# Kernel optimization log

Hardware: AMD Instinct MI355X
Metric: run time of the kernel (lower is better)

## Reference

```python
import jax, jax.numpy as jnp
import numpy as np

H, N2, R = 512, 16, 32   # hidden_dim, state_dim//2, dt_rank=ceil(512/16)
B, L = 1, 4096


def setup_inputs() -> dict:
    key = jax.random.key(0)
    ks = jax.random.split(key, 7)
    u = jax.random.normal(ks[0], (B, L, H), dtype=jnp.float32)
    # Parameter initialization mirroring S4DKernel.__init__
    A_log = jnp.zeros((H, N2), jnp.float32)                      # log(ones)
    A_im = jnp.broadcast_to(jnp.arange(N2, dtype=jnp.float32), (H, N2)).copy()
    B_param = jax.random.normal(ks[1], (H, N2, 2), jnp.float32)
    C_param = jax.random.normal(ks[2], (H, N2, 2), jnp.float32)
    D = jax.random.normal(ks[3], (H,), jnp.float32)
    dt_w = jax.random.normal(ks[4], (H, R), jnp.float32) / np.sqrt(R)
    dt_min, dt_max, dt_floor = 1e-3, 0.1, 1e-4
    dt_init = jnp.exp(jax.random.uniform(ks[5], (H,), jnp.float32)
                      * (np.log(dt_max) - np.log(dt_floor)) + np.log(dt_floor))
    dt_init = jnp.maximum(dt_init, dt_min)
    dt_b = dt_init + jnp.log(-jnp.expm1(-dt_init))               # inverse-softplus init
    xproj_w = jax.random.normal(ks[6], (R, H), jnp.float32) / np.sqrt(H)
    return {"u": u, "A_log": A_log, "A_im": A_im, "B_param": B_param,
            "C_param": C_param, "D": D, "dt_w": dt_w, "dt_b": dt_b,
            "xproj_w": xproj_w}


def reference(u, A_log, A_im, B_param, C_param, D, dt_w, dt_b, xproj_w):
    # Complex continuous-time parameters
    A = -jnp.exp(A_log) + 1j * A_im                 # [H, N2]
    Bc = B_param[..., 0] + 1j * B_param[..., 1]     # [H, N2]
    Cc = C_param[..., 0] + 1j * C_param[..., 1]     # [H, N2]

    # dt path: x_proj_for_dt (no bias) -> dt_proj -> softplus
    dt_u = jnp.einsum('blh,rh->blr', u, xproj_w)                    # [B,L,R]
    dt = jax.nn.softplus(jnp.einsum('blr,hr->blh', dt_u, dt_w) + dt_b)  # [B,L,H]

    # ZOH discretization
    z = dt[..., None] * A                           # [B,L,H,N2] complex
    A_bar = jnp.exp(z)
    B_bar_div = jnp.where(jnp.abs(z) < 1e-4, 1.0 + z / 2, (jnp.exp(z) - 1.0) / z)
    ub = u[..., None].astype(A_bar.dtype) * B_bar_div * Bc          # [B,L,H,N2]

    # Parallel scan for h_k = A_k * h_{k-1} + u_k (first-order linear recurrence)
    def op(c1, c2):
        a1, b1 = c1
        a2, b2 = c2
        return a1 * a2, a2 * b1 + b2
    _, h = jax.lax.associative_scan(op, (A_bar, ub), axis=1)        # [B,L,H,N2]

    y = jnp.einsum('blhn,hn->blh', h, Cc) + u * D
    return y.real
```

## Files before the change

### kernel.cpp

```cpp
#include <hip/hip_runtime.h>

#define Hd 512
#define N2d 16
#define Rd 32
#define Ld 4096
#define NCHUNK 128
#define CLEN (Ld / NCHUNK)
#define NCH (Hd * N2d)

__global__ __launch_bounds__(256) void k_tw(const float* __restrict__ dt_w,
                                            float* __restrict__ dt_wT) {
    int idx = blockIdx.x * 256 + threadIdx.x;
    int r = idx >> 9;
    int h = idx & 511;
    dt_wT[idx] = dt_w[h * Rd + r];
}

__global__ __launch_bounds__(256) void k_dt(const float* __restrict__ u,
                                            const float* __restrict__ xproj_w,
                                            const float* __restrict__ dt_wT,
                                            const float* __restrict__ dt_b,
                                            float2* __restrict__ du_out) {
    __shared__ float u_s[8][Hd];
    __shared__ float dtu_s[8][Rd];
    const int t = threadIdx.x;
    const int l0 = blockIdx.x * 8;

    #pragma unroll
    for (int i = 0; i < 16; ++i) {
        int idx = t + i * 256;
        ((float*)u_s)[idx] = u[l0 * Hd + idx];
    }
    __syncthreads();

    const int r = t >> 3;
    const int j = t & 7;
    float part[8];
    #pragma unroll
    for (int l = 0; l < 8; ++l) part[l] = 0.f;
    for (int k = 0; k < 64; ++k) {
        float w = xproj_w[r * Hd + k * 8 + j];
        #pragma unroll
        for (int l = 0; l < 8; ++l) part[l] = fmaf(u_s[l][k * 8 + j], w, part[l]);
    }
    #pragma unroll
    for (int off = 1; off < 8; off <<= 1) {
        #pragma unroll
        for (int l = 0; l < 8; ++l) part[l] += __shfl_xor(part[l], off);
    }
    if (j == 0) {
        #pragma unroll
        for (int l = 0; l < 8; ++l) dtu_s[l][r] = part[l];
    }
    __syncthreads();

    #pragma unroll
    for (int hb = 0; hb < 2; ++hb) {
        int h = hb * 256 + t;
        float bias = dt_b[h];
        float acc[8];
        #pragma unroll
        for (int l = 0; l < 8; ++l) acc[l] = bias;
        for (int rr = 0; rr < Rd; ++rr) {
            float w = dt_wT[rr * Hd + h];
            #pragma unroll
            for (int l = 0; l < 8; ++l) acc[l] = fmaf(dtu_s[l][rr], w, acc[l]);
        }
        #pragma unroll
        for (int l = 0; l < 8; ++l) {
            float x = acc[l];
            float sp = fmaxf(x, 0.f) + log1pf(__expf(-fabsf(x)));
            float uv = u_s[l][h];
            float us = uv * __builtin_amdgcn_rcpf(fmaxf(sp, 1e-30f));
            du_out[(l0 + l) * Hd + h] = make_float2(sp, us);
        }
    }
}

__device__ __forceinline__ bool load_consts4(const float* A_log, const float* A_im,
        const float* B_param, int hnb,
        float* Are, float* Aim, float* BAr, float* BAi) {
    #pragma unroll
    for (int j = 0; j < 4; ++j) {
        int hn = hnb + j;
        Are[j] = -__expf(A_log[hn]);
        Aim[j] = A_im[hn];
        float Bre = B_param[2 * hn];
        float Bim = B_param[2 * hn + 1];
        float inv = __builtin_amdgcn_rcpf(Are[j] * Are[j] + Aim[j] * Aim[j]);
        BAr[j] = (Bre * Are[j] + Bim * Aim[j]) * inv;
        BAi[j] = (Bim * Are[j] - Bre * Aim[j]) * inv;
    }
    float d1 = Aim[1] - Aim[0], d2 = Aim[2] - Aim[1], d3 = Aim[3] - Aim[2];
    return (Are[1] == Are[0]) && (Are[2] == Are[0]) && (Are[3] == Are[0]) &&
           (d1 == d2) && (d2 == d3);
}

__global__ __launch_bounds__(256) void k_chunk(const float2* __restrict__ du,
        const float* __restrict__ A_log, const float* __restrict__ A_im,
        const float* __restrict__ B_param,
        float2* __restrict__ Pbuf, float2* __restrict__ Sbuf) {
    const int t = threadIdx.x;
    const int q = t & 3;
    const int h = blockIdx.y * 64 + (t >> 2);
    const int c = blockIdx.x;
    const int hnb = h * N2d + q * 4;
    float Are[4], Aim[4], BAr[4], BAi[4];
    const bool fast = load_consts4(A_log, A_im, B_param, hnb, Are, Aim, BAr, BAi);
    float sr[4] = {0.f, 0.f, 0.f, 0.f}, si[4] = {0.f, 0.f, 0.f, 0.f};
    float sdt = 0.f;
    const int lbase = c * CLEN;
    if (fast) {
        const float Are0 = Are[0], Aim0 = Aim[0], dA = Aim[1] - Aim[0];
        #pragma unroll 4
        for (int k = 0; k < CLEN; ++k) {
            float2 d = du[(lbase + k) * Hd + h];
            float dtv = d.x, us = d.y;
            sdt += dtv;
            float er = __expf(dtv * Are0);
            float s0, c0, sd, cd;
            __sincosf(dtv * Aim0, &s0, &c0);
            __sincosf(dtv * dA, &sd, &cd);
            float ar = er * c0, ai = er * s0;
            #pragma unroll
            for (int j = 0; j < 4; ++j) {
                float gr = fmaf(ar, us, -us);
                float gi = ai * us;
                float nr = fmaf(ar, sr[j], fmaf(-ai, si[j], fmaf(gr, BAr[j], -gi * BAi[j])));
                float ni = fmaf(ar, si[j], fmaf( ai, sr[j], fmaf(gr, BAi[j],  gi * BAr[j])));
                sr[j] = nr; si[j] = ni;
                if (j < 3) {
                    float tr = fmaf(ar, cd, -ai * sd);
                    ai = fmaf(ai, cd, ar * sd);
                    ar = tr;
                }
            }
        }
    } else {
        #pragma unroll 4
        for (int k = 0; k < CLEN; ++k) {
            float2 d = du[(lbase + k) * Hd + h];
            float dtv = d.x, us = d.y;
            sdt += dtv;
            #pragma unroll
            for (int j = 0; j < 4; ++j) {
                float er = __expf(dtv * Are[j]);
                float s, cc;
                __sincosf(dtv * Aim[j], &s, &cc);
                float ar = er * cc, ai = er * s;
                float gr = fmaf(ar, us, -us);
                float gi = ai * us;
                float nr = fmaf(ar, sr[j], fmaf(-ai, si[j], fmaf(gr, BAr[j], -gi * BAi[j])));
                float ni = fmaf(ar, si[j], fmaf( ai, sr[j], fmaf(gr, BAi[j],  gi * BAr[j])));
                sr[j] = nr; si[j] = ni;
            }
        }
    }
    int base = c * NCH + hnb;
    #pragma unroll
    for (int j = 0; j < 4; ++j) {
        float er = __expf(sdt * Are[j]);
        float s, cc;
        __sincosf(sdt * Aim[j], &s, &cc);
        Pbuf[base + j] = make_float2(er * cc, er * s);
        Sbuf[base + j] = make_float2(sr[j], si[j]);
    }
}

__global__ __launch_bounds__(256) void k_prefix(const float2* __restrict__ Pbuf,
        const float2* __restrict__ Sbuf, float2* __restrict__ Ibuf) {
    int idx = blockIdx.x * 256 + threadIdx.x;
    float hr = 0.f, hi = 0.f;
    for (int b = 0; b < NCHUNK / 8; ++b) {
        float2 tp[8], ts[8];
        #pragma unroll
        for (int i = 0; i < 8; ++i) {
            tp[i] = Pbuf[(b * 8 + i) * NCH + idx];
            ts[i] = Sbuf[(b * 8 + i) * NCH + idx];
        }
        #pragma unroll
        for (int i = 0; i < 8; ++i) {
            Ibuf[(b * 8 + i) * NCH + idx] = make_float2(hr, hi);
            float nr = fmaf(tp[i].x, hr, fmaf(-tp[i].y, hi, ts[i].x));
            float ni = fmaf(tp[i].x, hi, fmaf( tp[i].y, hr, ts[i].y));
            hr = nr; hi = ni;
        }
    }
}

__global__ __launch_bounds__(256) void k_scan(const float2* __restrict__ du,
        const float* __restrict__ A_log, const float* __restrict__ A_im,
        const float* __restrict__ B_param, const float* __restrict__ C_param,
        const float* __restrict__ Dp, const float2* __restrict__ Ibuf,
        float* __restrict__ out) {
    const int t = threadIdx.x;
    const int q = t & 3;
    const int h = blockIdx.y * 64 + (t >> 2);
    const int c = blockIdx.x;
    const int hnb = h * N2d + q * 4;
    float Are[4], Aim[4], BAr[4], BAi[4], Cre[4], Cim[4];
    const bool fast = load_consts4(A_log, A_im, B_param, hnb, Are, Aim, BAr, BAi);
    #pragma unroll
    for (int j = 0; j < 4; ++j) {
        Cre[j] = C_param[2 * (hnb + j)];
        Cim[j] = C_param[2 * (hnb + j) + 1];
    }
    const float Dv = Dp[h];
    float hr[4], hi[4];
    {
        int base = c * NCH + hnb;
        #pragma unroll
        for (int j = 0; j < 4; ++j) {
            float2 h0 = Ibuf[base + j];
            hr[j] = h0.x; hi[j] = h0.y;
        }
    }
    const int lbase = c * CLEN;
    if (fast) {
        const float Are0 = Are[0], Aim0 = Aim[0], dA = Aim[1] - Aim[0];
        #pragma unroll 4
        for (int k = 0; k < CLEN; ++k) {
            int l = lbase + k;
            float2 d = du[l * Hd + h];
            float dtv = d.x, us = d.y;
            float er = __expf(dtv * Are0);
            float s0, c0, sd, cd;
            __sincosf(dtv * Aim0, &s0, &c0);
            __sincosf(dtv * dA, &sd, &cd);
            float ar = er * c0, ai = er * s0;
            float yv = 0.f;
            #pragma unroll
            for (int j = 0; j < 4; ++j) {
                float gr = fmaf(ar, us, -us);
                float gi = ai * us;
                float nr = fmaf(ar, hr[j], fmaf(-ai, hi[j], fmaf(gr, BAr[j], -gi * BAi[j])));
                float ni = fmaf(ar, hi[j], fmaf( ai, hr[j], fmaf(gr, BAi[j],  gi * BAr[j])));
                hr[j] = nr; hi[j] = ni;
                yv = fmaf(nr, Cre[j], fmaf(-ni, Cim[j], yv));
                if (j < 3) {
                    float tr = fmaf(ar, cd, -ai * sd);
                    ai = fmaf(ai, cd, ar * sd);
                    ar = tr;
                }
            }
            yv += __shfl_xor(yv, 1);
            yv += __shfl_xor(yv, 2);
            if (q == 0) out[l * Hd + h] = fmaf(dtv * us, Dv, yv);
        }
    } else {
        #pragma unroll 4
        for (int k = 0; k < CLEN; ++k) {
            int l = lbase + k;
            float2 d = du[l * Hd + h];
            float dtv = d.x, us = d.y;
            float yv = 0.f;
            #pragma unroll
            for (int j = 0; j < 4; ++j) {
                float er = __expf(dtv * Are[j]);
                float s, cc;
                __sincosf(dtv * Aim[j], &s, &cc);
                float ar = er * cc, ai = er * s;
                float gr = fmaf(ar, us, -us);
                float gi = ai * us;
                float nr = fmaf(ar, hr[j], fmaf(-ai, hi[j], fmaf(gr, BAr[j], -gi * BAi[j])));
                float ni = fmaf(ar, hi[j], fmaf( ai, hr[j], fmaf(gr, BAi[j],  gi * BAr[j])));
                hr[j] = nr; hi[j] = ni;
                yv = fmaf(nr, Cre[j], fmaf(-ni, Cim[j], yv));
            }
            yv += __shfl_xor(yv, 1);
            yv += __shfl_xor(yv, 2);
            if (q == 0) out[l * Hd + h] = fmaf(dtv * us, Dv, yv);
        }
    }
}

extern "C" void kernel_launch(void* const* d_in, const int* in_sizes, int n_in,
                              void* d_out, int out_size, void* d_ws, size_t ws_size,
                              hipStream_t stream) {
    const float* u        = (const float*)d_in[0];
    const float* A_log    = (const float*)d_in[1];
    const float* A_im     = (const float*)d_in[2];
    const float* B_param  = (const float*)d_in[3];
    const float* C_param  = (const float*)d_in[4];
    const float* Dp       = (const float*)d_in[5];
    const float* dt_w     = (const float*)d_in[6];
    const float* dt_b     = (const float*)d_in[7];
    const float* xproj_w  = (const float*)d_in[8];

    float2* du   = (float2*)d_ws;
    float2* Pbuf = du + (size_t)Ld * Hd;
    float2* Sbuf = Pbuf + (size_t)NCHUNK * NCH;
    float2* Ibuf = Sbuf + (size_t)NCHUNK * NCH;
    float*  dt_wT = (float*)(Ibuf + (size_t)NCHUNK * NCH);
    float*  out  = (float*)d_out;

    k_tw<<<(Rd * Hd) / 256, 256, 0, stream>>>(dt_w, dt_wT);
    k_dt<<<Ld / 8, 256, 0, stream>>>(u, xproj_w, dt_wT, dt_b, du);
    dim3 g2(NCHUNK, Hd / 64);
    k_chunk<<<g2, 256, 0, stream>>>(du, A_log, A_im, B_param, Pbuf, Sbuf);
    k_prefix<<<NCH / 256, 256, 0, stream>>>(Pbuf, Sbuf, Ibuf);
    k_scan<<<g2, 256, 0, stream>>>(du, A_log, A_im, B_param, C_param, Dp, Ibuf, out);
}
```

Before: 154.3 us.

## Replace second chunk rescan with local outputs plus carried-state correction

The chunk pass now also emits per-step local outputs (zero initial state) and cumulative dt within the chunk. The final scan kernel is replaced by a fully parallel correction kernel that adds C·exp(A·T)·h_in, using the prefix-propagated carry already multiplied by C. This removes the second sequential recurrence pass over each chunk. In exchange it writes and reads a 4x-wide y4 buffer plus a T buffer, about 40 MB of extra traffic, and recomputes exponentials per (l,h).

```diff
diff --git a/kernel.cpp b/kernel.cpp
--- a/kernel.cpp
+++ b/kernel.cpp
@@ -14,6 +14,22 @@
     int r = idx >> 9;
     int h = idx & 511;
     dt_wT[idx] = dt_w[h * Rd + r];
+}
+
+__global__ __launch_bounds__(256) void k_hinfo(const float* __restrict__ A_log,
+                                               const float* __restrict__ A_im,
+                                               float4* __restrict__ hinfo) {
+    int h = blockIdx.x * 256 + threadIdx.x;
+    if (h >= Hd) return;
+    float Are0 = -__expf(A_log[h * N2d]);
+    float Aim0 = A_im[h * N2d];
+    float dA = A_im[h * N2d + 1] - Aim0;
+    bool ok = true;
+    for (int j = 1; j < N2d; ++j) {
+        float a = -__expf(A_log[h * N2d + j]);
+        ok = ok && (a == Are0) && (A_im[h * N2d + j] == Aim0 + j * dA);
+    }
+    hinfo[h] = make_float4(Are0, Aim0, dA, ok ? 1.f : 0.f);
 }
 
 __global__ __launch_bounds__(256) void k_dt(const float* __restrict__ u,
@@ -98,15 +114,23 @@
 
 __global__ __launch_bounds__(256) void k_chunk(const float2* __restrict__ du,
         const float* __restrict__ A_log, const float* __restrict__ A_im,
-        const float* __restrict__ B_param,
-        float2* __restrict__ Pbuf, float2* __restrict__ Sbuf) {
+        const float* __restrict__ B_param, const float* __restrict__ C_param,
+        const float* __restrict__ Dp,
+        float2* __restrict__ Pbuf, float2* __restrict__ Sbuf,
+        float* __restrict__ y4, float* __restrict__ T) {
     const int t = threadIdx.x;
     const int q = t & 3;
     const int h = blockIdx.y * 64 + (t >> 2);
     const int c = blockIdx.x;
     const int hnb = h * N2d + q * 4;
-    float Are[4], Aim[4], BAr[4], BAi[4];
+    float Are[4], Aim[4], BAr[4], BAi[4], Cre[4], Cim[4];
     const bool fast = load_consts4(A_log, A_im, B_param, hnb, Are, Aim, BAr, BAi);
+    #pragma unroll
+    for (int j = 0; j < 4; ++j) {
+        Cre[j] = C_param[2 * (hnb + j)];
+        Cim[j] = C_param[2 * (hnb + j) + 1];
+    }
+    const float Dv = Dp[h];
     float sr[4] = {0.f, 0.f, 0.f, 0.f}, si[4] = {0.f, 0.f, 0.f, 0.f};
     float sdt = 0.f;
     const int lbase = c * CLEN;
@@ -114,7 +138,8 @@
         const float Are0 = Are[0], Aim0 = Aim[0], dA = Aim[1] - Aim[0];
         #pragma unroll 4
         for (int k = 0; k < CLEN; ++k) {
-            float2 d = du[(lbase + k) * Hd + h];
+            int l = lbase + k;
+            float2 d = du[l * Hd + h];
             float dtv = d.x, us = d.y;
             sdt += dtv;
             float er = __expf(dtv * Are0);
@@ -122,6 +147,7 @@
             __sincosf(dtv * Aim0, &s0, &c0);
             __sincosf(dtv * dA, &sd, &cd);
             float ar = er * c0, ai = er * s0;
+            float yq = 0.f;
             #pragma unroll
             for (int j = 0; j < 4; ++j) {
                 float gr = fmaf(ar, us, -us);
@@ -129,19 +155,27 @@
                 float nr = fmaf(ar, sr[j], fmaf(-ai, si[j], fmaf(gr, BAr[j], -gi * BAi[j])));
                 float ni = fmaf(ar, si[j], fmaf( ai, sr[j], fmaf(gr, BAi[j],  gi * BAr[j])));
                 sr[j] = nr; si[j] = ni;
+                yq = fmaf(nr, Cre[j], fmaf(-ni, Cim[j], yq));
                 if (j < 3) {
                     float tr = fmaf(ar, cd, -ai * sd);
                     ai = fmaf(ai, cd, ar * sd);
                     ar = tr;
                 }
             }
+            if (q == 0) {
+                yq = fmaf(dtv * us, Dv, yq);
+                T[l * Hd + h] = sdt;
+            }
+            y4[((l * Hd + h) << 2) | q] = yq;
         }
     } else {
         #pragma unroll 4
         for (int k = 0; k < CLEN; ++k) {
-            float2 d = du[(lbase + k) * Hd + h];
+            int l = lbase + k;
+            float2 d = du[l * Hd + h];
             float dtv = d.x, us = d.y;
             sdt += dtv;
+            float yq = 0.f;
             #pragma unroll
             for (int j = 0; j < 4; ++j) {
                 float er = __expf(dtv * Are[j]);
@@ -153,7 +187,13 @@
                 float nr = fmaf(ar, sr[j], fmaf(-ai, si[j], fmaf(gr, BAr[j], -gi * BAi[j])));
                 float ni = fmaf(ar, si[j], fmaf( ai, sr[j], fmaf(gr, BAi[j],  gi * BAr[j])));
                 sr[j] = nr; si[j] = ni;
+                yq = fmaf(nr, Cre[j], fmaf(-ni, Cim[j], yq));
             }
+            if (q == 0) {
+                yq = fmaf(dtv * us, Dv, yq);
+                T[l * Hd + h] = sdt;
+            }
+            y4[((l * Hd + h) << 2) | q] = yq;
         }
     }
     int base = c * NCH + hnb;
@@ -168,8 +208,11 @@
 }
 
 __global__ __launch_bounds__(256) void k_prefix(const float2* __restrict__ Pbuf,
-        const float2* __restrict__ Sbuf, float2* __restrict__ Ibuf) {
+        const float2* __restrict__ Sbuf, const float* __restrict__ C_param,
+        float2* __restrict__ Gbuf) {
     int idx = blockIdx.x * 256 + threadIdx.x;
+    float Cre = C_param[2 * idx];
+    float Cim = C_param[2 * idx + 1];
     float hr = 0.f, hi = 0.f;
     for (int b = 0; b < NCHUNK / 8; ++b) {
         float2 tp[8], ts[8];
@@ -180,7 +223,8 @@
         }
         #pragma unroll
         for (int i = 0; i < 8; ++i) {
-            Ibuf[(b * 8 + i) * NCH + idx] = make_float2(hr, hi);
+            Gbuf[(b * 8 + i) * NCH + idx] =
+                make_float2(fmaf(Cre, hr, -Cim * hi), fmaf(Cre, hi, Cim * hr));
             float nr = fmaf(tp[i].x, hr, fmaf(-tp[i].y, hi, ts[i].x));
             float ni = fmaf(tp[i].x, hi, fmaf( tp[i].y, hr, ts[i].y));
             hr = nr; hi = ni;
@@ -188,90 +232,53 @@
     }
 }
 
-__global__ __launch_bounds__(256) void k_scan(const float2* __restrict__ du,
-        const float* __restrict__ A_log, const float* __restrict__ A_im,
-        const float* __restrict__ B_param, const float* __restrict__ C_param,
-        const float* __restrict__ Dp, const float2* __restrict__ Ibuf,
-        float* __restrict__ out) {
-    const int t = threadIdx.x;
-    const int q = t & 3;
-    const int h = blockIdx.y * 64 + (t >> 2);
-    const int c = blockIdx.x;
-    const int hnb = h * N2d + q * 4;
-    float Are[4], Aim[4], BAr[4], BAi[4], Cre[4], Cim[4];
-    const bool fast = load_consts4(A_log, A_im, B_param, hnb, Are, Aim, BAr, BAi);
-    #pragma unroll
-    for (int j = 0; j < 4; ++j) {
-        Cre[j] = C_param[2 * (hnb + j)];
-        Cim[j] = C_param[2 * (hnb + j) + 1];
-    }
-    const float Dv = Dp[h];
-    float hr[4], hi[4];
-    {
-        int base = c * NCH + hnb;
-        #pragma unroll
-        for (int j = 0; j < 4; ++j) {
-            float2 h0 = Ibuf[base + j];
-            hr[j] = h0.x; hi[j] = h0.y;
-        }
-    }
-    const int lbase = c * CLEN;
-    if (fast) {
-        const float Are0 = Are[0], Aim0 = Aim[0], dA = Aim[1] - Aim[0];
+__global__ __launch_bounds__(256) void k_corr(const float* __restrict__ y4,
+        const float* __restrict__ T, const float2* __restrict__ Gbuf,
+        const float4* __restrict__ hinfo, const float* __restrict__ A_log,
+        const float* __restrict__ A_im, float* __restrict__ out) {
+    int gid = blockIdx.x * 256 + threadIdx.x;
+    int l = gid >> 9;
+    int h = gid & 511;
+    int c = l / CLEN;
+    float4 yv = ((const float4*)y4)[gid];
+    float ysum = (yv.x + yv.y) + (yv.z + yv.w);
+    float Tv = T[gid];
+    float4 hi4 = hinfo[h];
+    const float4* G4 = (const float4*)(Gbuf + (size_t)c * NCH + h * N2d);
+    float acc = 0.f;
+    if (hi4.w != 0.f) {
+        float er = __expf(Tv * hi4.x);
+        float s0, c0, sd, cd;
+        __sincosf(Tv * hi4.y, &s0, &c0);
+        __sincosf(Tv * hi4.z, &sd, &cd);
+        float rr = c0, ri = s0;
+        #pragma unroll
+        for (int j = 0; j < 8; ++j) {
+            float4 g = G4[j];
+            acc = fmaf(g.x, rr, fmaf(-g.y, ri, acc));
+            float tr = fmaf(rr, cd, -ri * sd);
+            ri = fmaf(ri, cd, rr * sd);
+            rr = tr;
+            acc = fmaf(g.z, rr, fmaf(-g.w, ri, acc));
+            tr = fmaf(rr, cd, -ri * sd);
+            ri = fmaf(ri, cd, rr * sd);
+            rr = tr;
+        }
+        acc *= er;
+    } else {
+        const float2* G2 = (const float2*)G4;
         #pragma unroll 4
-        for (int k = 0; k < CLEN; ++k) {
-            int l = lbase + k;
-            float2 d = du[l * Hd + h];
-            float dtv = d.x, us = d.y;
-            float er = __expf(dtv * Are0);
-            float s0, c0, sd, cd;
-            __sincosf(dtv * Aim0, &s0, &c0);
-            __sincosf(dtv * dA, &sd, &cd);
-            float ar = er * c0, ai = er * s0;
-            float yv = 0.f;
-            #pragma unroll
-            for (int j = 0; j < 4; ++j) {
-                float gr = fmaf(ar, us, -us);
-                float gi = ai * us;
-                float nr = fmaf(ar, hr[j], fmaf(-ai, hi[j], fmaf(gr, BAr[j], -gi * BAi[j])));
-                float ni = fmaf(ar, hi[j], fmaf( ai, hr[j], fmaf(gr, BAi[j],  gi * BAr[j])));
-                hr[j] = nr; hi[j] = ni;
-                yv = fmaf(nr, Cre[j], fmaf(-ni, Cim[j], yv));
-                if (j < 3) {
-                    float tr = fmaf(ar, cd, -ai * sd);
-                    ai = fmaf(ai, cd, ar * sd);
-                    ar = tr;
-                }
-            }
-            yv += __shfl_xor(yv, 1);
-            yv += __shfl_xor(yv, 2);
-            if (q == 0) out[l * Hd + h] = fmaf(dtv * us, Dv, yv);
-        }
-    } else {
-        #pragma unroll 4
-        for (int k = 0; k < CLEN; ++k) {
-            int l = lbase + k;
-            float2 d = du[l * Hd + h];
-            float dtv = d.x, us = d.y;
-            float yv = 0.f;
-            #pragma unroll
-            for (int j = 0; j < 4; ++j) {
-                float er = __expf(dtv * Are[j]);
-                float s, cc;
-                __sincosf(dtv * Aim[j], &s, &cc);
-                float ar = er * cc, ai = er * s;
-                float gr = fmaf(ar, us, -us);
-                float gi = ai * us;
-                float nr = fmaf(ar, hr[j], fmaf(-ai, hi[j], fmaf(gr, BAr[j], -gi * BAi[j])));
-                float ni = fmaf(ar, hi[j], fmaf( ai, hr[j], fmaf(gr, BAi[j],  gi * BAr[j])));
-                hr[j] = nr; hi[j] = ni;
-                yv = fmaf(nr, Cre[j], fmaf(-ni, Cim[j], yv));
-            }
-            yv += __shfl_xor(yv, 1);
-            yv += __shfl_xor(yv, 2);
-            if (q == 0) out[l * Hd + h] = fmaf(dtv * us, Dv, yv);
-        }
-    }
+        for (int j = 0; j < N2d; ++j) {
+            int hn = h * N2d + j;
+            float Are = -__expf(A_log[hn]);
+            float er = __expf(Tv * Are);
+            float s, cc;
+            __sincosf(Tv * A_im[hn], &s, &cc);
+            float2 g = G2[j];
+            acc = fmaf(g.x * er, cc, fmaf(-g.y * er, s, acc));
+        }
+    }
+    out[gid] = ysum + acc;
 }
 
 extern "C" void kernel_launch(void* const* d_in, const int* in_sizes, int n_in,
@@ -290,14 +297,20 @@
     float2* du   = (float2*)d_ws;
     float2* Pbuf = du + (size_t)Ld * Hd;
     float2* Sbuf = Pbuf + (size_t)NCHUNK * NCH;
-    float2* Ibuf = Sbuf + (size_t)NCHUNK * NCH;
-    float*  dt_wT = (float*)(Ibuf + (size_t)NCHUNK * NCH);
+    float2* Gbuf = Sbuf + (size_t)NCHUNK * NCH;
+    float*  y4   = (float*)(Gbuf + (size_t)NCHUNK * NCH);
+    float*  T    = y4 + (size_t)Ld * Hd * 4;
+    float*  dt_wT = T + (size_t)Ld * Hd;
+    float4* hinfo = (float4*)(dt_wT + Rd * Hd);
     float*  out  = (float*)d_out;
 
     k_tw<<<(Rd * Hd) / 256, 256, 0, stream>>>(dt_w, dt_wT);
+    k_hinfo<<<2, 256, 0, stream>>>(A_log, A_im, hinfo);
     k_dt<<<Ld / 8, 256, 0, stream>>>(u, xproj_w, dt_wT, dt_b, du);
     dim3 g2(NCHUNK, Hd / 64);
-    k_chunk<<<g2, 256, 0, stream>>>(du, A_log, A_im, B_param, Pbuf, Sbuf);
-    k_prefix<<<NCH / 256, 256, 0, stream>>>(Pbuf, Sbuf, Ibuf);
-    k_scan<<<g2, 256, 0, stream>>>(du, A_log, A_im, B_param, C_param, Dp, Ibuf, out);
-}
+    k_chunk<<<g2, 256, 0, stream>>>(du, A_log, A_im, B_param, C_param, Dp,
+                                    Pbuf, Sbuf, y4, T);
+    k_prefix<<<NCH / 256, 256, 0, stream>>>(Pbuf, Sbuf, C_param, Gbuf);
+    k_corr<<<(Ld * Hd) / 256, 256, 0, stream>>>(y4, T, Gbuf, hinfo,
+                                                A_log, A_im, out);
+}
```

New measurement: 170.6 us. 10.6% more time.

## Map one thread per channel with all 16 states and double chunk count

Applied to the files above, without the earlier changes.

Each thread in the chunk and scan kernels now handles one hidden channel and all 16 states, instead of four threads sharing a channel with four states each. This removes the shuffle reduction and reuses one exp/sincos set across 16 states through the rotation recurrence. The chunk count is doubled to keep enough blocks, and the chunk decay and state are packed into a single float4 buffer with a state-major layout so prefix-kernel loads coalesce. The costs are much higher register pressure from 16-wide state arrays, fewer threads per chunk, and a longer serial prefix over 256 chunks.

```diff
diff --git a/kernel.cpp b/kernel.cpp
--- a/kernel.cpp
+++ b/kernel.cpp
@@ -4,7 +4,7 @@
 #define N2d 16
 #define Rd 32
 #define Ld 4096
-#define NCHUNK 128
+#define NCHUNK 256
 #define CLEN (Ld / NCHUNK)
 #define NCH (Hd * N2d)
 
@@ -77,42 +77,44 @@
     }
 }
 
-__device__ __forceinline__ bool load_consts4(const float* A_log, const float* A_im,
-        const float* B_param, int hnb,
-        float* Are, float* Aim, float* BAr, float* BAi) {
-    #pragma unroll
-    for (int j = 0; j < 4; ++j) {
-        int hn = hnb + j;
-        Are[j] = -__expf(A_log[hn]);
-        Aim[j] = A_im[hn];
-        float Bre = B_param[2 * hn];
-        float Bim = B_param[2 * hn + 1];
-        float inv = __builtin_amdgcn_rcpf(Are[j] * Are[j] + Aim[j] * Aim[j]);
-        BAr[j] = (Bre * Are[j] + Bim * Aim[j]) * inv;
-        BAi[j] = (Bim * Are[j] - Bre * Aim[j]) * inv;
-    }
-    float d1 = Aim[1] - Aim[0], d2 = Aim[2] - Aim[1], d3 = Aim[3] - Aim[2];
-    return (Are[1] == Are[0]) && (Are[2] == Are[0]) && (Are[3] == Are[0]) &&
-           (d1 == d2) && (d2 == d3);
+__device__ __forceinline__ bool setup_h(const float* __restrict__ A_log,
+        const float* __restrict__ A_im, const float* __restrict__ B_param,
+        int h, float& Are0, float& Aim0, float& dA,
+        float* __restrict__ BAr, float* __restrict__ BAi) {
+    const int hb = h * N2d;
+    Are0 = -__expf(A_log[hb]);
+    Aim0 = A_im[hb];
+    dA = A_im[hb + 1] - Aim0;
+    bool ok = true;
+    #pragma unroll
+    for (int j = 0; j < N2d; ++j) {
+        int hn = hb + j;
+        float Ar = -__expf(A_log[hn]);
+        float Ai = A_im[hn];
+        ok = ok && (Ar == Are0) && (Ai == fmaf((float)j, dA, Aim0));
+        float Br = B_param[2 * hn];
+        float Bi = B_param[2 * hn + 1];
+        float inv = __builtin_amdgcn_rcpf(Ar * Ar + Ai * Ai);
+        BAr[j] = (Br * Ar + Bi * Ai) * inv;
+        BAi[j] = (Bi * Ar - Br * Ai) * inv;
+    }
+    return ok;
 }
 
 __global__ __launch_bounds__(256) void k_chunk(const float2* __restrict__ du,
         const float* __restrict__ A_log, const float* __restrict__ A_im,
-        const float* __restrict__ B_param,
-        float2* __restrict__ Pbuf, float2* __restrict__ Sbuf) {
-    const int t = threadIdx.x;
-    const int q = t & 3;
-    const int h = blockIdx.y * 64 + (t >> 2);
+        const float* __restrict__ B_param, float4* __restrict__ PS) {
+    const int h = blockIdx.y * 256 + threadIdx.x;
     const int c = blockIdx.x;
-    const int hnb = h * N2d + q * 4;
-    float Are[4], Aim[4], BAr[4], BAi[4];
-    const bool fast = load_consts4(A_log, A_im, B_param, hnb, Are, Aim, BAr, BAi);
-    float sr[4] = {0.f, 0.f, 0.f, 0.f}, si[4] = {0.f, 0.f, 0.f, 0.f};
+    float Are0, Aim0, dA, BAr[N2d], BAi[N2d];
+    const bool fast = setup_h(A_log, A_im, B_param, h, Are0, Aim0, dA, BAr, BAi);
+    float sr[N2d], si[N2d];
+    #pragma unroll
+    for (int j = 0; j < N2d; ++j) { sr[j] = 0.f; si[j] = 0.f; }
     float sdt = 0.f;
     const int lbase = c * CLEN;
     if (fast) {
-        const float Are0 = Are[0], Aim0 = Aim[0], dA = Aim[1] - Aim[0];
-        #pragma unroll 4
+        #pragma unroll 2
         for (int k = 0; k < CLEN; ++k) {
             float2 d = du[(lbase + k) * Hd + h];
             float dtv = d.x, us = d.y;
@@ -123,30 +125,42 @@
             __sincosf(dtv * dA, &sd, &cd);
             float ar = er * c0, ai = er * s0;
             #pragma unroll
-            for (int j = 0; j < 4; ++j) {
+            for (int j = 0; j < N2d; ++j) {
                 float gr = fmaf(ar, us, -us);
                 float gi = ai * us;
                 float nr = fmaf(ar, sr[j], fmaf(-ai, si[j], fmaf(gr, BAr[j], -gi * BAi[j])));
                 float ni = fmaf(ar, si[j], fmaf( ai, sr[j], fmaf(gr, BAi[j],  gi * BAr[j])));
                 sr[j] = nr; si[j] = ni;
-                if (j < 3) {
+                if (j < N2d - 1) {
                     float tr = fmaf(ar, cd, -ai * sd);
                     ai = fmaf(ai, cd, ar * sd);
                     ar = tr;
                 }
             }
         }
+        float er = __expf(sdt * Are0);
+        float s0, c0, sd, cd;
+        __sincosf(sdt * Aim0, &s0, &c0);
+        __sincosf(sdt * dA, &sd, &cd);
+        float pr = er * c0, pi = er * s0;
+        #pragma unroll
+        for (int j = 0; j < N2d; ++j) {
+            PS[c * NCH + j * Hd + h] = make_float4(pr, pi, sr[j], si[j]);
+            float tr = fmaf(pr, cd, -pi * sd);
+            pi = fmaf(pi, cd, pr * sd);
+            pr = tr;
+        }
     } else {
-        #pragma unroll 4
         for (int k = 0; k < CLEN; ++k) {
             float2 d = du[(lbase + k) * Hd + h];
             float dtv = d.x, us = d.y;
             sdt += dtv;
             #pragma unroll
-            for (int j = 0; j < 4; ++j) {
-                float er = __expf(dtv * Are[j]);
+            for (int j = 0; j < N2d; ++j) {
+                int hn = h * N2d + j;
+                float er = __expf(dtv * -__expf(A_log[hn]));
                 float s, cc;
-                __sincosf(dtv * Aim[j], &s, &cc);
+                __sincosf(dtv * A_im[hn], &s, &cc);
                 float ar = er * cc, ai = er * s;
                 float gr = fmaf(ar, us, -us);
                 float gi = ai * us;
@@ -155,34 +169,30 @@
                 sr[j] = nr; si[j] = ni;
             }
         }
-    }
-    int base = c * NCH + hnb;
-    #pragma unroll
-    for (int j = 0; j < 4; ++j) {
-        float er = __expf(sdt * Are[j]);
-        float s, cc;
-        __sincosf(sdt * Aim[j], &s, &cc);
-        Pbuf[base + j] = make_float2(er * cc, er * s);
-        Sbuf[base + j] = make_float2(sr[j], si[j]);
-    }
-}
-
-__global__ __launch_bounds__(256) void k_prefix(const float2* __restrict__ Pbuf,
-        const float2* __restrict__ Sbuf, float2* __restrict__ Ibuf) {
+        #pragma unroll
+        for (int j = 0; j < N2d; ++j) {
+            int hn = h * N2d + j;
+            float er = __expf(sdt * -__expf(A_log[hn]));
+            float s, cc;
+            __sincosf(sdt * A_im[hn], &s, &cc);
+            PS[c * NCH + j * Hd + h] = make_float4(er * cc, er * s, sr[j], si[j]);
+        }
+    }
+}
+
+__global__ __launch_bounds__(256) void k_prefix(const float4* __restrict__ PS,
+                                                float2* __restrict__ Ibuf) {
     int idx = blockIdx.x * 256 + threadIdx.x;
     float hr = 0.f, hi = 0.f;
-    for (int b = 0; b < NCHUNK / 8; ++b) {
-        float2 tp[8], ts[8];
-        #pragma unroll
-        for (int i = 0; i < 8; ++i) {
-            tp[i] = Pbuf[(b * 8 + i) * NCH + idx];
-            ts[i] = Sbuf[(b * 8 + i) * NCH + idx];
-        }
-        #pragma unroll
-        for (int i = 0; i < 8; ++i) {
-            Ibuf[(b * 8 + i) * NCH + idx] = make_float2(hr, hi);
-            float nr = fmaf(tp[i].x, hr, fmaf(-tp[i].y, hi, ts[i].x));
-            float ni = fmaf(tp[i].x, hi, fmaf( tp[i].y, hr, ts[i].y));
+    for (int b = 0; b < NCHUNK / 16; ++b) {
+        float4 tp[16];
+        #pragma unroll
+        for (int i = 0; i < 16; ++i) tp[i] = PS[(b * 16 + i) * NCH + idx];
+        #pragma unroll
+        for (int i = 0; i < 16; ++i) {
+            Ibuf[(b * 16 + i) * NCH + idx] = make_float2(hr, hi);
+            float nr = fmaf(tp[i].x, hr, fmaf(-tp[i].y, hi, tp[i].z));
+            float ni = fmaf(tp[i].x, hi, fmaf( tp[i].y, hr, tp[i].w));
             hr = nr; hi = ni;
         }
     }
@@ -193,32 +203,26 @@
         const float* __restrict__ B_param, const float* __restrict__ C_param,
         const float* __restrict__ Dp, const float2* __restrict__ Ibuf,
         float* __restrict__ out) {
-    const int t = threadIdx.x;
-    const int q = t & 3;
-    const int h = blockIdx.y * 64 + (t >> 2);
+    const int h = blockIdx.y * 256 + threadIdx.x;
     const int c = blockIdx.x;
-    const int hnb = h * N2d + q * 4;
-    float Are[4], Aim[4], BAr[4], BAi[4], Cre[4], Cim[4];
-    const bool fast = load_consts4(A_log, A_im, B_param, hnb, Are, Aim, BAr, BAi);
-    #pragma unroll
-    for (int j = 0; j < 4; ++j) {
-        Cre[j] = C_param[2 * (hnb + j)];
-        Cim[j] = C_param[2 * (hnb + j) + 1];
+    float Are0, Aim0, dA, BAr[N2d], BAi[N2d];
+    const bool fast = setup_h(A_log, A_im, B_param, h, Are0, Aim0, dA, BAr, BAi);
+    float Cre[N2d], Cim[N2d];
+    #pragma unroll
+    for (int j = 0; j < N2d; ++j) {
+        Cre[j] = C_param[2 * (h * N2d + j)];
+        Cim[j] = C_param[2 * (h * N2d + j) + 1];
     }
     const float Dv = Dp[h];
-    float hr[4], hi[4];
-    {
-        int base = c * NCH + hnb;
-        #pragma unroll
-        for (int j = 0; j < 4; ++j) {
-            float2 h0 = Ibuf[base + j];
-            hr[j] = h0.x; hi[j] = h0.y;
-        }
+    float sr[N2d], si[N2d];
+    #pragma unroll
+    for (int j = 0; j < N2d; ++j) {
+        float2 h0 = Ibuf[c * NCH + j * Hd + h];
+        sr[j] = h0.x; si[j] = h0.y;
     }
     const int lbase = c * CLEN;
     if (fast) {
-        const float Are0 = Are[0], Aim0 = Aim[0], dA = Aim[1] - Aim[0];
-        #pragma unroll 4
+        #pragma unroll 2
         for (int k = 0; k < CLEN; ++k) {
             int l = lbase + k;
             float2 d = du[l * Hd + h];
@@ -230,46 +234,42 @@
             float ar = er * c0, ai = er * s0;
             float yv = 0.f;
             #pragma unroll
-            for (int j = 0; j < 4; ++j) {
+            for (int j = 0; j < N2d; ++j) {
                 float gr = fmaf(ar, us, -us);
                 float gi = ai * us;
-                float nr = fmaf(ar, hr[j], fmaf(-ai, hi[j], fmaf(gr, BAr[j], -gi * BAi[j])));
-                float ni = fmaf(ar, hi[j], fmaf( ai, hr[j], fmaf(gr, BAi[j],  gi * BAr[j])));
-                hr[j] = nr; hi[j] = ni;
+                float nr = fmaf(ar, sr[j], fmaf(-ai, si[j], fmaf(gr, BAr[j], -gi * BAi[j])));
+                float ni = fmaf(ar, si[j], fmaf( ai, sr[j], fmaf(gr, BAi[j],  gi * BAr[j])));
+                sr[j] = nr; si[j] = ni;
                 yv = fmaf(nr, Cre[j], fmaf(-ni, Cim[j], yv));
-                if (j < 3) {
+                if (j < N2d - 1) {
                     float tr = fmaf(ar, cd, -ai * sd);
                     ai = fmaf(ai, cd, ar * sd);
                     ar = tr;
                 }
             }
-            yv += __shfl_xor(yv, 1);
-            yv += __shfl_xor(yv, 2);
-            if (q == 0) out[l * Hd + h] = fmaf(dtv * us, Dv, yv);
+            out[l * Hd + h] = fmaf(dtv * us, Dv, yv);
         }
     } else {
-        #pragma unroll 4
         for (int k = 0; k < CLEN; ++k) {
             int l = lbase + k;
             float2 d = du[l * Hd + h];
             float dtv = d.x, us = d.y;
             float yv = 0.f;
             #pragma unroll
-            for (int j = 0; j < 4; ++j) {
-                float er = __expf(dtv * Are[j]);
+            for (int j = 0; j < N2d; ++j) {
+                int hn = h * N2d + j;
+                float er = __expf(dtv * -__expf(A_log[hn]));
                 float s, cc;
-                __sincosf(dtv * Aim[j], &s, &cc);
+                __sincosf(dtv * A_im[hn], &s, &cc);
                 float ar = er * cc, ai = er * s;
                 float gr = fmaf(ar, us, -us);
                 float gi = ai * us;
-                float nr = fmaf(ar, hr[j], fmaf(-ai, hi[j], fmaf(gr, BAr[j], -gi * BAi[j])));
-                float ni = fmaf(ar, hi[j], fmaf( ai, hr[j], fmaf(gr, BAi[j],  gi * BAr[j])));
-                hr[j] = nr; hi[j] = ni;
+                float nr = fmaf(ar, sr[j], fmaf(-ai, si[j], fmaf(gr, BAr[j], -gi * BAi[j])));
+                float ni = fmaf(ar, si[j], fmaf( ai, sr[j], fmaf(gr, BAi[j],  gi * BAr[j])));
+                sr[j] = nr; si[j] = ni;
                 yv = fmaf(nr, Cre[j], fmaf(-ni, Cim[j], yv));
             }
-            yv += __shfl_xor(yv, 1);
-            yv += __shfl_xor(yv, 2);
-            if (q == 0) out[l * Hd + h] = fmaf(dtv * us, Dv, yv);
+            out[l * Hd + h] = fmaf(dtv * us, Dv, yv);
         }
     }
 }
@@ -288,16 +288,15 @@
     const float* xproj_w  = (const float*)d_in[8];
 
     float2* du   = (float2*)d_ws;
-    float2* Pbuf = du + (size_t)Ld * Hd;
-    float2* Sbuf = Pbuf + (size_t)NCHUNK * NCH;
-    float2* Ibuf = Sbuf + (size_t)NCHUNK * NCH;
+    float4* PS   = (float4*)(du + (size_t)Ld * Hd);
+    float2* Ibuf = (float2*)(PS + (size_t)NCHUNK * NCH);
     float*  dt_wT = (float*)(Ibuf + (size_t)NCHUNK * NCH);
     float*  out  = (float*)d_out;
 
     k_tw<<<(Rd * Hd) / 256, 256, 0, stream>>>(dt_w, dt_wT);
     k_dt<<<Ld / 8, 256, 0, stream>>>(u, xproj_w, dt_wT, dt_b, du);
-    dim3 g2(NCHUNK, Hd / 64);
-    k_chunk<<<g2, 256, 0, stream>>>(du, A_log, A_im, B_param, Pbuf, Sbuf);
-    k_prefix<<<NCH / 256, 256, 0, stream>>>(Pbuf, Sbuf, Ibuf);
+    dim3 g2(NCHUNK, Hd / 256);
+    k_chunk<<<g2, 256, 0, stream>>>(du, A_log, A_im, B_param, PS);
+    k_prefix<<<NCH / 256, 256, 0, stream>>>(PS, Ibuf);
     k_scan<<<g2, 256, 0, stream>>>(du, A_log, A_im, B_param, C_param, Dp, Ibuf, out);
 }
```

Measured after the change: 167.8 us. 8.8% more time.

## Split dt/u workspace, pack chunk state into float4, double chunk count

Applied to the files above, without the earlier changes.

Stores the softplus dt and the scaled input as two separate float arrays instead of interleaved float2 pairs. Chunk decay and chunk state are packed into one float4 buffer laid out state-major with h innermost, so chunk writes and scan reads are coalesced. The number of chunks doubles, giving the scan kernels more parallel blocks at the cost of a longer serial prefix pass. It also halves the rows per k_dt block, computes the fast-path chunk decay with a rotation recurrence instead of per-state sincos, and replaces log1pf with __logf(1+e), which loses a little precision.

```diff
diff --git a/kernel.cpp b/kernel.cpp
--- a/kernel.cpp
+++ b/kernel.cpp
@@ -4,7 +4,7 @@
 #define N2d 16
 #define Rd 32
 #define Ld 4096
-#define NCHUNK 128
+#define NCHUNK 256
 #define CLEN (Ld / NCHUNK)
 #define NCH (Hd * N2d)
 
@@ -20,14 +20,15 @@
                                             const float* __restrict__ xproj_w,
                                             const float* __restrict__ dt_wT,
                                             const float* __restrict__ dt_b,
-                                            float2* __restrict__ du_out) {
-    __shared__ float u_s[8][Hd];
-    __shared__ float dtu_s[8][Rd];
+                                            float* __restrict__ dtp,
+                                            float* __restrict__ usp) {
+    __shared__ float u_s[4][Hd];
+    __shared__ float dtu_s[4][Rd];
     const int t = threadIdx.x;
-    const int l0 = blockIdx.x * 8;
-
-    #pragma unroll
-    for (int i = 0; i < 16; ++i) {
+    const int l0 = blockIdx.x * 4;
+
+    #pragma unroll
+    for (int i = 0; i < 8; ++i) {
         int idx = t + i * 256;
         ((float*)u_s)[idx] = u[l0 * Hd + idx];
     }
@@ -35,22 +36,20 @@
 
     const int r = t >> 3;
     const int j = t & 7;
-    float part[8];
-    #pragma unroll
-    for (int l = 0; l < 8; ++l) part[l] = 0.f;
+    float part[4] = {0.f, 0.f, 0.f, 0.f};
     for (int k = 0; k < 64; ++k) {
         float w = xproj_w[r * Hd + k * 8 + j];
         #pragma unroll
-        for (int l = 0; l < 8; ++l) part[l] = fmaf(u_s[l][k * 8 + j], w, part[l]);
+        for (int l = 0; l < 4; ++l) part[l] = fmaf(u_s[l][k * 8 + j], w, part[l]);
     }
     #pragma unroll
     for (int off = 1; off < 8; off <<= 1) {
         #pragma unroll
-        for (int l = 0; l < 8; ++l) part[l] += __shfl_xor(part[l], off);
+        for (int l = 0; l < 4; ++l) part[l] += __shfl_xor(part[l], off);
     }
     if (j == 0) {
         #pragma unroll
-        for (int l = 0; l < 8; ++l) dtu_s[l][r] = part[l];
+        for (int l = 0; l < 4; ++l) dtu_s[l][r] = part[l];
     }
     __syncthreads();
 
@@ -58,48 +57,49 @@
     for (int hb = 0; hb < 2; ++hb) {
         int h = hb * 256 + t;
         float bias = dt_b[h];
-        float acc[8];
-        #pragma unroll
-        for (int l = 0; l < 8; ++l) acc[l] = bias;
+        float acc[4] = {bias, bias, bias, bias};
         for (int rr = 0; rr < Rd; ++rr) {
             float w = dt_wT[rr * Hd + h];
             #pragma unroll
-            for (int l = 0; l < 8; ++l) acc[l] = fmaf(dtu_s[l][rr], w, acc[l]);
-        }
-        #pragma unroll
-        for (int l = 0; l < 8; ++l) {
+            for (int l = 0; l < 4; ++l) acc[l] = fmaf(dtu_s[l][rr], w, acc[l]);
+        }
+        #pragma unroll
+        for (int l = 0; l < 4; ++l) {
             float x = acc[l];
-            float sp = fmaxf(x, 0.f) + log1pf(__expf(-fabsf(x)));
+            float e = __expf(-fabsf(x));
+            float sp = fmaxf(x, 0.f) + __logf(1.f + e);
             float uv = u_s[l][h];
             float us = uv * __builtin_amdgcn_rcpf(fmaxf(sp, 1e-30f));
-            du_out[(l0 + l) * Hd + h] = make_float2(sp, us);
-        }
-    }
-}
-
-__device__ __forceinline__ bool load_consts4(const float* A_log, const float* A_im,
-        const float* B_param, int hnb,
-        float* Are, float* Aim, float* BAr, float* BAi) {
+            dtp[(l0 + l) * Hd + h] = sp;
+            usp[(l0 + l) * Hd + h] = us;
+        }
+    }
+}
+
+__device__ __forceinline__ bool load_consts4(const float* __restrict__ A_log,
+        const float* __restrict__ A_im, const float* __restrict__ B_param,
+        int hnb, float* __restrict__ Are, float* __restrict__ Aim,
+        float* __restrict__ BAr, float* __restrict__ BAi) {
     #pragma unroll
     for (int j = 0; j < 4; ++j) {
         int hn = hnb + j;
         Are[j] = -__expf(A_log[hn]);
         Aim[j] = A_im[hn];
-        float Bre = B_param[2 * hn];
-        float Bim = B_param[2 * hn + 1];
+        float Br = B_param[2 * hn];
+        float Bi = B_param[2 * hn + 1];
         float inv = __builtin_amdgcn_rcpf(Are[j] * Are[j] + Aim[j] * Aim[j]);
-        BAr[j] = (Bre * Are[j] + Bim * Aim[j]) * inv;
-        BAi[j] = (Bim * Are[j] - Bre * Aim[j]) * inv;
+        BAr[j] = (Br * Are[j] + Bi * Aim[j]) * inv;
+        BAi[j] = (Bi * Are[j] - Br * Aim[j]) * inv;
     }
     float d1 = Aim[1] - Aim[0], d2 = Aim[2] - Aim[1], d3 = Aim[3] - Aim[2];
     return (Are[1] == Are[0]) && (Are[2] == Are[0]) && (Are[3] == Are[0]) &&
            (d1 == d2) && (d2 == d3);
 }
 
-__global__ __launch_bounds__(256) void k_chunk(const float2* __restrict__ du,
+__global__ __launch_bounds__(256) void k_chunk(const float* __restrict__ dtp,
+        const float* __restrict__ usp,
         const float* __restrict__ A_log, const float* __restrict__ A_im,
-        const float* __restrict__ B_param,
-        float2* __restrict__ Pbuf, float2* __restrict__ Sbuf) {
+        const float* __restrict__ B_param, float4* __restrict__ PS) {
     const int t = threadIdx.x;
     const int q = t & 3;
     const int h = blockIdx.y * 64 + (t >> 2);
@@ -109,17 +109,18 @@
     const bool fast = load_consts4(A_log, A_im, B_param, hnb, Are, Aim, BAr, BAi);
     float sr[4] = {0.f, 0.f, 0.f, 0.f}, si[4] = {0.f, 0.f, 0.f, 0.f};
     float sdt = 0.f;
-    const int lbase = c * CLEN;
+    const float* dp = dtp + (size_t)c * CLEN * Hd + h;
+    const float* up = usp + (size_t)c * CLEN * Hd + h;
     if (fast) {
-        const float Are0 = Are[0], Aim0 = Aim[0], dA = Aim[1] - Aim[0];
+        const float Are0 = Are[0], Aimb = Aim[0], dA = Aim[1] - Aim[0];
         #pragma unroll 4
         for (int k = 0; k < CLEN; ++k) {
-            float2 d = du[(lbase + k) * Hd + h];
-            float dtv = d.x, us = d.y;
+            float dtv = dp[k * Hd];
+            float us  = up[k * Hd];
             sdt += dtv;
             float er = __expf(dtv * Are0);
             float s0, c0, sd, cd;
-            __sincosf(dtv * Aim0, &s0, &c0);
+            __sincosf(dtv * Aimb, &s0, &c0);
             __sincosf(dtv * dA, &sd, &cd);
             float ar = er * c0, ai = er * s0;
             #pragma unroll
@@ -136,11 +137,23 @@
                 }
             }
         }
+        float er = __expf(sdt * Are0);
+        float s0, c0, sd, cd;
+        __sincosf(sdt * Aimb, &s0, &c0);
+        __sincosf(sdt * dA, &sd, &cd);
+        float pr = er * c0, pi = er * s0;
+        #pragma unroll
+        for (int j = 0; j < 4; ++j) {
+            PS[c * NCH + (hnb + j - h * N2d) * Hd + h + (h * N2d / N2d) * 0] =
+                make_float4(pr, pi, sr[j], si[j]);
+            float tr = fmaf(pr, cd, -pi * sd);
+            pi = fmaf(pi, cd, pr * sd);
+            pr = tr;
+        }
     } else {
-        #pragma unroll 4
         for (int k = 0; k < CLEN; ++k) {
-            float2 d = du[(lbase + k) * Hd + h];
-            float dtv = d.x, us = d.y;
+            float dtv = dp[k * Hd];
+            float us  = up[k * Hd];
             sdt += dtv;
             #pragma unroll
             for (int j = 0; j < 4; ++j) {
@@ -155,40 +168,36 @@
                 sr[j] = nr; si[j] = ni;
             }
         }
-    }
-    int base = c * NCH + hnb;
-    #pragma unroll
-    for (int j = 0; j < 4; ++j) {
-        float er = __expf(sdt * Are[j]);
-        float s, cc;
-        __sincosf(sdt * Aim[j], &s, &cc);
-        Pbuf[base + j] = make_float2(er * cc, er * s);
-        Sbuf[base + j] = make_float2(sr[j], si[j]);
-    }
-}
-
-__global__ __launch_bounds__(256) void k_prefix(const float2* __restrict__ Pbuf,
-        const float2* __restrict__ Sbuf, float2* __restrict__ Ibuf) {
+        #pragma unroll
+        for (int j = 0; j < 4; ++j) {
+            float er = __expf(sdt * Are[j]);
+            float s, cc;
+            __sincosf(sdt * Aim[j], &s, &cc);
+            PS[c * NCH + (q * 4 + j) * Hd + h] = make_float4(er * cc, er * s, sr[j], si[j]);
+        }
+    }
+}
+
+__global__ __launch_bounds__(256) void k_prefix(const float4* __restrict__ PS,
+                                                float2* __restrict__ Ibuf) {
     int idx = blockIdx.x * 256 + threadIdx.x;
     float hr = 0.f, hi = 0.f;
-    for (int b = 0; b < NCHUNK / 8; ++b) {
-        float2 tp[8], ts[8];
-        #pragma unroll
-        for (int i = 0; i < 8; ++i) {
-            tp[i] = Pbuf[(b * 8 + i) * NCH + idx];
-            ts[i] = Sbuf[(b * 8 + i) * NCH + idx];
-        }
-        #pragma unroll
-        for (int i = 0; i < 8; ++i) {
-            Ibuf[(b * 8 + i) * NCH + idx] = make_float2(hr, hi);
-            float nr = fmaf(tp[i].x, hr, fmaf(-tp[i].y, hi, ts[i].x));
-            float ni = fmaf(tp[i].x, hi, fmaf( tp[i].y, hr, ts[i].y));
+    for (int b = 0; b < NCHUNK / 16; ++b) {
+        float4 tp[16];
+        #pragma unroll
+        for (int i = 0; i < 16; ++i) tp[i] = PS[(b * 16 + i) * NCH + idx];
+        #pragma unroll
+        for (int i = 0; i < 16; ++i) {
+            Ibuf[(b * 16 + i) * NCH + idx] = make_float2(hr, hi);
+            float nr = fmaf(tp[i].x, hr, fmaf(-tp[i].y, hi, tp[i].z));
+            float ni = fmaf(tp[i].x, hi, fmaf( tp[i].y, hr, tp[i].w));
             hr = nr; hi = ni;
         }
     }
 }
 
-__global__ __launch_bounds__(256) void k_scan(const float2* __restrict__ du,
+__global__ __launch_bounds__(256) void k_scan(const float* __restrict__ dtp,
+        const float* __restrict__ usp,
         const float* __restrict__ A_log, const float* __restrict__ A_im,
         const float* __restrict__ B_param, const float* __restrict__ C_param,
         const float* __restrict__ Dp, const float2* __restrict__ Ibuf,
@@ -206,26 +215,24 @@
         Cim[j] = C_param[2 * (hnb + j) + 1];
     }
     const float Dv = Dp[h];
-    float hr[4], hi[4];
-    {
-        int base = c * NCH + hnb;
-        #pragma unroll
-        for (int j = 0; j < 4; ++j) {
-            float2 h0 = Ibuf[base + j];
-            hr[j] = h0.x; hi[j] = h0.y;
-        }
-    }
-    const int lbase = c * CLEN;
+    float sr[4], si[4];
+    #pragma unroll
+    for (int j = 0; j < 4; ++j) {
+        float2 h0 = Ibuf[c * NCH + (q * 4 + j) * Hd + h];
+        sr[j] = h0.x; si[j] = h0.y;
+    }
+    const float* dp = dtp + (size_t)c * CLEN * Hd + h;
+    const float* up = usp + (size_t)c * CLEN * Hd + h;
+    float* op = out + (size_t)c * CLEN * Hd + h;
     if (fast) {
-        const float Are0 = Are[0], Aim0 = Aim[0], dA = Aim[1] - Aim[0];
+        const float Are0 = Are[0], Aimb = Aim[0], dA = Aim[1] - Aim[0];
         #pragma unroll 4
         for (int k = 0; k < CLEN; ++k) {
-            int l = lbase + k;
-            float2 d = du[l * Hd + h];
-            float dtv = d.x, us = d.y;
+            float dtv = dp[k * Hd];
+            float us  = up[k * Hd];
             float er = __expf(dtv * Are0);
             float s0, c0, sd, cd;
-            __sincosf(dtv * Aim0, &s0, &c0);
+            __sincosf(dtv * Aimb, &s0, &c0);
             __sincosf(dtv * dA, &sd, &cd);
             float ar = er * c0, ai = er * s0;
             float yv = 0.f;
@@ -233,9 +240,9 @@
             for (int j = 0; j < 4; ++j) {
                 float gr = fmaf(ar, us, -us);
                 float gi = ai * us;
-                float nr = fmaf(ar, hr[j], fmaf(-ai, hi[j], fmaf(gr, BAr[j], -gi * BAi[j])));
-                float ni = fmaf(ar, hi[j], fmaf( ai, hr[j], fmaf(gr, BAi[j],  gi * BAr[j])));
-                hr[j] = nr; hi[j] = ni;
+                float nr = fmaf(ar, sr[j], fmaf(-ai, si[j], fmaf(gr, BAr[j], -gi * BAi[j])));
+                float ni = fmaf(ar, si[j], fmaf( ai, sr[j], fmaf(gr, BAi[j],  gi * BAr[j])));
+                sr[j] = nr; si[j] = ni;
                 yv = fmaf(nr, Cre[j], fmaf(-ni, Cim[j], yv));
                 if (j < 3) {
                     float tr = fmaf(ar, cd, -ai * sd);
@@ -245,14 +252,12 @@
             }
             yv += __shfl_xor(yv, 1);
             yv += __shfl_xor(yv, 2);
-            if (q == 0) out[l * Hd + h] = fmaf(dtv * us, Dv, yv);
+            if (q == 0) op[k * Hd] = fmaf(dtv * us, Dv, yv);
         }
     } else {
-        #pragma unroll 4
         for (int k = 0; k < CLEN; ++k) {
-            int l = lbase + k;
-            float2 d = du[l * Hd + h];
-            float dtv = d.x, us = d.y;
+            float dtv = dp[k * Hd];
+            float us  = up[k * Hd];
             float yv = 0.f;
             #pragma unroll
             for (int j = 0; j < 4; ++j) {
@@ -262,14 +267,14 @@
                 float ar = er * cc, ai = er * s;
                 float gr = fmaf(ar, us, -us);
                 float gi = ai * us;
-                float nr = fmaf(ar, hr[j], fmaf(-ai, hi[j], fmaf(gr, BAr[j], -gi * BAi[j])));
-                float ni = fmaf(ar, hi[j], fmaf( ai, hr[j], fmaf(gr, BAi[j],  gi * BAr[j])));
-                hr[j] = nr; hi[j] = ni;
+                float nr = fmaf(ar, sr[j], fmaf(-ai, si[j], fmaf(gr, BAr[j], -gi * BAi[j])));
+                float ni = fmaf(ar, si[j], fmaf( ai, sr[j], fmaf(gr, BAi[j],  gi * BAr[j])));
+                sr[j] = nr; si[j] = ni;
                 yv = fmaf(nr, Cre[j], fmaf(-ni, Cim[j], yv));
             }
             yv += __shfl_xor(yv, 1);
             yv += __shfl_xor(yv, 2);
-            if (q == 0) out[l * Hd + h] = fmaf(dtv * us, Dv, yv);
+            if (q == 0) op[k * Hd] = fmaf(dtv * us, Dv, yv);
         }
     }
 }
@@ -287,17 +292,18 @@
     const float* dt_b     = (const float*)d_in[7];
     const float* xproj_w  = (const float*)d_in[8];
 
-    float2* du   = (float2*)d_ws;
-    float2* Pbuf = du + (size_t)Ld * Hd;
-    float2* Sbuf = Pbuf + (size_t)NCHUNK * NCH;
-    float2* Ibuf = Sbuf + (size_t)NCHUNK * NCH;
+    float*  dtp  = (float*)d_ws;
+    float*  usp  = dtp + (size_t)Ld * Hd;
+    float4* PS   = (float4*)(usp + (size_t)Ld * Hd);
+    float2* Ibuf = (float2*)(PS + (size_t)NCHUNK * NCH);
     float*  dt_wT = (float*)(Ibuf + (size_t)NCHUNK * NCH);
     float*  out  = (float*)d_out;
 
     k_tw<<<(Rd * Hd) / 256, 256, 0, stream>>>(dt_w, dt_wT);
-    k_dt<<<Ld / 8, 256, 0, stream>>>(u, xproj_w, dt_wT, dt_b, du);
+    k_dt<<<Ld / 4, 256, 0, stream>>>(u, xproj_w, dt_wT, dt_b, dtp, usp);
     dim3 g2(NCHUNK, Hd / 64);
-    k_chunk<<<g2, 256, 0, stream>>>(du, A_log, A_im, B_param, Pbuf, Sbuf);
-    k_prefix<<<NCH / 256, 256, 0, stream>>>(Pbuf, Sbuf, Ibuf);
-    k_scan<<<g2, 256, 0, stream>>>(du, A_log, A_im, B_param, C_param, Dp, Ibuf, out);
-}
+    k_chunk<<<g2, 256, 0, stream>>>(dtp, usp, A_log, A_im, B_param, PS);
+    k_prefix<<<NCH / 256, 256, 0, stream>>>(PS, Ibuf);
+    k_scan<<<g2, 256, 0, stream>>>(dtp, usp, A_log, A_im, B_param, C_param,
+                                   Dp, Ibuf, out);
+}
```

Measured after the change: 162.6 us. +5.4%, slower.
